# Kernel optimization log

Measured on AMD Instinct MI355X. Metric: run time of the kernel, lower is better.

## Reference

```python
import jax, jax.numpy as jnp
import numpy as np

D_MODEL = 768
H = 12
D_FF = 3072
EPS = 1e-6


def _layernorm(x, alpha, bias):
    # torch.std default is Bessel-corrected (ddof=1); denom is (std + eps)
    mean = jnp.mean(x, axis=-1, keepdims=True)
    var = jnp.sum((x - mean) ** 2, axis=-1, keepdims=True) / (x.shape[-1] - 1)
    std = jnp.sqrt(var)
    return alpha * (x - mean) / (std + EPS) + bias


def _linear(x, w, b):
    # torch nn.Linear: y = x @ W.T + b, W is [out, in]
    return jnp.einsum('...i,oi->...o', x, w) + b


def setup_inputs() -> dict:
    key = jax.random.key(0)
    ks = jax.random.split(key, 16)
    B, S = 8, 1024
    sc = 1.0 / np.sqrt(D_MODEL)
    inp = {
        'x': jax.random.normal(ks[0], (B, S, D_MODEL), dtype=jnp.float32),
        'mask': jax.random.randint(ks[1], (B, 1, 1, S), 0, 2, dtype=jnp.int32),
        'wq': jax.random.normal(ks[2], (D_MODEL, D_MODEL), dtype=jnp.float32) * sc,
        'bq': jnp.zeros((D_MODEL,), jnp.float32),
        'wk': jax.random.normal(ks[3], (D_MODEL, D_MODEL), dtype=jnp.float32) * sc,
        'bk': jnp.zeros((D_MODEL,), jnp.float32),
        'wv': jax.random.normal(ks[4], (D_MODEL, D_MODEL), dtype=jnp.float32) * sc,
        'bv': jnp.zeros((D_MODEL,), jnp.float32),
        'wo': jax.random.normal(ks[5], (D_MODEL, D_MODEL), dtype=jnp.float32) * sc,
        'bo': jnp.zeros((D_MODEL,), jnp.float32),
        'ln1_a': jnp.ones((D_MODEL,), jnp.float32),
        'ln1_b': jnp.zeros((D_MODEL,), jnp.float32),
        'ln2_a': jnp.ones((D_MODEL,), jnp.float32),
        'ln2_b': jnp.zeros((D_MODEL,), jnp.float32),
        'w1': jax.random.normal(ks[6], (D_FF, D_MODEL), dtype=jnp.float32) * sc,
        'b1': jnp.zeros((D_FF,), jnp.float32),
        'w2': jax.random.normal(ks[7], (D_MODEL, D_FF), dtype=jnp.float32) * (1.0 / np.sqrt(D_FF)),
        'b2': jnp.zeros((D_MODEL,), jnp.float32),
    }
    return inp


def reference(x, mask, wq, bq, wk, bk, wv, bv, wo, bo,
              ln1_a, ln1_b, ln2_a, ln2_b, w1, b1, w2, b2):
    B, S, _ = x.shape
    d_k = D_MODEL // H

    # --- residual 1: pre-LN self-attention (dropout identity at eval) ---
    xn = _layernorm(x, ln1_a, ln1_b)
    q = _linear(xn, wq, bq).reshape(B, S, H, d_k).transpose(0, 2, 1, 3)
    k = _linear(xn, wk, bk).reshape(B, S, H, d_k).transpose(0, 2, 1, 3)
    v = _linear(xn, wv, bv).reshape(B, S, H, d_k).transpose(0, 2, 1, 3)

    scores = jnp.einsum('bhqd,bhkd->bhqk', q, k) / jnp.sqrt(jnp.float32(d_k))
    # faithful quirk: masked positions set to 1e-9, NOT -inf
    scores = jnp.where(mask == 0, jnp.float32(1e-9), scores)
    attn = jax.nn.softmax(scores, axis=-1)
    ctx = jnp.einsum('bhqk,bhkd->bhqd', attn, v)
    ctx = ctx.transpose(0, 2, 1, 3).reshape(B, S, D_MODEL)
    x = x + _linear(ctx, wo, bo)

    # --- residual 2: pre-LN feed-forward ---
    xn = _layernorm(x, ln2_a, ln2_b)
    ff = _linear(jax.nn.relu(_linear(xn, w1, b1)), w2, b2)
    return x + ff
```

## Files before the change

### kernel.cpp

```cpp
#include <hip/hip_runtime.h>
#include <stdint.h>

#define D_MODEL 768
#define D_FF    3072
#define NH      12
#define DK      64
#define BB      8
#define SS      1024
#define NTOK    (BB*SS)
#define QST     2304

typedef float          f32x4  __attribute__((ext_vector_type(4)));
typedef __bf16         bf16x8 __attribute__((ext_vector_type(8)));
typedef unsigned short us8v   __attribute__((ext_vector_type(8)));
typedef unsigned short us4v   __attribute__((ext_vector_type(4)));

__device__ __forceinline__ unsigned short f2b(float f) {
  unsigned int u = __builtin_bit_cast(unsigned int, f);
  u = (u + 0x7fffu + ((u >> 16) & 1u)) >> 16;
  return (unsigned short)u;
}
__device__ __forceinline__ float b2f(unsigned short h) {
  unsigned int u = ((unsigned int)h) << 16;
  return __builtin_bit_cast(float, u);
}
__device__ __forceinline__ float exp2a(float x) {
  float r; asm("v_exp_f32 %0, %1" : "=v"(r) : "v"(x)); return r;
}
__device__ __forceinline__ unsigned int cvtpk(float lo, float hi) {
  unsigned int r;
  asm("v_cvt_pk_bf16_f32 %0, %1, %2" : "=v"(r) : "v"(lo), "v"(hi));
  return r;
}

#define N4TOT 1769472
__global__ __launch_bounds__(256) void cast6_kernel(
    const float* __restrict__ s0, const float* __restrict__ s1,
    const float* __restrict__ s2, const float* __restrict__ s3,
    const float* __restrict__ s4, const float* __restrict__ s5,
    unsigned short* __restrict__ d0, unsigned short* __restrict__ d1,
    unsigned short* __restrict__ d2, unsigned short* __restrict__ d3,
    unsigned short* __restrict__ d4, unsigned short* __restrict__ d5) {
  int i = blockIdx.x * 256 + threadIdx.x;
  if (i >= N4TOT) return;
  const float* src; unsigned short* dst; int off;
  if (i < 147456)       { src = s0; dst = d0; off = i; }
  else if (i < 294912)  { src = s1; dst = d1; off = i - 147456; }
  else if (i < 442368)  { src = s2; dst = d2; off = i - 294912; }
  else if (i < 589824)  { src = s3; dst = d3; off = i - 442368; }
  else if (i < 1179648) { src = s4; dst = d4; off = i - 589824; }
  else                  { src = s5; dst = d5; off = i - 1179648; }
  float4 f = ((const float4*)src)[off];
  us4v o; o.x = f2b(f.x); o.y = f2b(f.y); o.z = f2b(f.z); o.w = f2b(f.w);
  *(us4v*)(dst + (size_t)off * 4) = o;
}

__global__ __launch_bounds__(256) void ln_kernel(const float* __restrict__ x,
                                                 const float* __restrict__ ga,
                                                 const float* __restrict__ gb,
                                                 unsigned short* __restrict__ y) {
  int row = blockIdx.x;
  const float* xr = x + (size_t)row * D_MODEL;
  int t = threadIdx.x, w = t >> 6, l = t & 63;
  float v0 = xr[t], v1 = xr[t + 256], v2 = xr[t + 512];
  float s = v0 + v1 + v2;
  #pragma unroll
  for (int off = 32; off; off >>= 1) s += __shfl_xor(s, off);
  __shared__ float red[4];
  __shared__ float stats[2];
  if (l == 0) red[w] = s;
  __syncthreads();
  if (t == 0) stats[0] = (red[0] + red[1] + red[2] + red[3]) * (1.0f / 768.0f);
  __syncthreads();
  float mean = stats[0];
  float d0 = v0 - mean, d1 = v1 - mean, d2 = v2 - mean;
  float ss = d0 * d0 + d1 * d1 + d2 * d2;
  #pragma unroll
  for (int off = 32; off; off >>= 1) ss += __shfl_xor(ss, off);
  __syncthreads();
  if (l == 0) red[w] = ss;
  __syncthreads();
  if (t == 0) {
    float tot = red[0] + red[1] + red[2] + red[3];
    stats[1] = 1.0f / (sqrtf(tot * (1.0f / 767.0f)) + 1e-6f);
  }
  __syncthreads();
  float inv = stats[1];
  unsigned short* yr = y + (size_t)row * D_MODEL;
  yr[t]       = f2b(ga[t]       * (d0 * inv) + gb[t]);
  yr[t + 256] = f2b(ga[t + 256] * (d1 * inv) + gb[t + 256]);
  yr[t + 512] = f2b(ga[t + 512] * (d2 * inv) + gb[t + 512]);
}

#define GLDS(g, l) __builtin_amdgcn_global_load_lds( \
    (__attribute__((address_space(1))) const void*)(g), \
    (__attribute__((address_space(3))) void*)(l), 16, 0, 0)

template<int BN>
__global__ __launch_bounds__(256) void gemm_t(
    const unsigned short* __restrict__ A,
    const unsigned short* __restrict__ W,
    const float* __restrict__ biasA,
    const float* __restrict__ biasB,
    const float* __restrict__ biasC,
    int segw,
    const float* __restrict__ resid,
    float* __restrict__ outF,
    unsigned short* __restrict__ outB,
    int M, int N, int K, int relu) {
  constexpr int BK  = (BN == 128) ? 32 : 64;
  constexpr int WC  = (BN == 128) ? 2 : 1;
  constexpr int MF  = (BN == 128) ? 4 : 2;
  constexpr int NF  = 4;
  constexpr int ASZ = 128 * BK;
  constexpr int BSZ = BN * BK;
  __shared__ unsigned short As[2 * ASZ];
  __shared__ unsigned short Bs[2 * BSZ];
  int t = threadIdx.x;
  int w = t >> 6, l = t & 63;
  int brow = blockIdx.x * 128;
  int bcol = blockIdx.y * BN;
  int wr = (w / WC) * (MF * 16);
  int wc = (w % WC) * (NF * 16);

  const unsigned short *ga0, *ga1, *gb0, *gb1;
  if constexpr (BN == 128) {
    ga0 = A + (size_t)(brow + (t >> 2)) * K + (t & 3) * 8;
    ga1 = ga0 + (size_t)64 * K;
    gb0 = W + (size_t)(bcol + (t >> 2)) * K + (t & 3) * 8;
    gb1 = gb0 + (size_t)64 * K;
  } else {
    int r5 = t >> 3;
    int swz = (t & 7) ^ (r5 & 7);
    ga0 = A + (size_t)(brow + r5) * K + swz * 8;
    gb0 = W + (size_t)(bcol + r5) * K + swz * 8;
    ga1 = gb1 = nullptr;
  }

  f32x4 acc[MF][NF];
  #pragma unroll
  for (int m = 0; m < MF; m++)
    #pragma unroll
    for (int n = 0; n < NF; n++)
      acc[m][n] = (f32x4){0.f, 0.f, 0.f, 0.f};

  int arow = wr + (l & 15);
  int bcw  = wc + (l & 15);
  int g    = l >> 4;
  int kk   = g * 8;
  const int nt = K / BK;

  auto stage = [&](int ti, int buf) {
    int k0 = ti * BK;
    if constexpr (BN == 128) {
      GLDS(ga0 + k0, As + buf * ASZ + t * 8);
      GLDS(ga1 + k0, As + buf * ASZ + 2048 + t * 8);
      GLDS(gb0 + k0, Bs + buf * BSZ + t * 8);
      GLDS(gb1 + k0, Bs + buf * BSZ + 2048 + t * 8);
    } else {
      #pragma unroll
      for (int i = 0; i < 4; i++)
        GLDS(ga0 + k0 + (size_t)(32 * i) * K, As + buf * ASZ + i * 2048 + t * 8);
      #pragma unroll
      for (int i = 0; i < 2; i++)
        GLDS(gb0 + k0 + (size_t)(32 * i) * K, Bs + buf * BSZ + i * 2048 + t * 8);
    }
  };

  stage(0, 0);
  __syncthreads();

  int cb = 0;
  for (int ti = 0; ti < nt; ti++) {
    if (ti + 1 < nt) stage(ti + 1, cb ^ 1);
    #pragma unroll
    for (int h = 0; h < BK / 32; h++) {
      bf16x8 af[MF], bfv[NF];
      #pragma unroll
      for (int m = 0; m < MF; m++) {
        int aro = arow + m * 16;
        if constexpr (BN == 128)
          af[m] = *(const bf16x8*)(As + cb * ASZ + aro * 32 + kk);
        else
          af[m] = *(const bf16x8*)(As + cb * ASZ + aro * 64 +
                                   ((((h << 2) + g) ^ (l & 7)) << 3));
      }
      #pragma unroll
      for (int n = 0; n < NF; n++) {
        int bco = bcw + n * 16;
        if constexpr (BN == 128)
          bfv[n] = *(const bf16x8*)(Bs + cb * BSZ + bco * 32 + kk);
        else
          bfv[n] = *(const bf16x8*)(Bs + cb * BSZ + bco * 64 +
                                    ((((h << 2) + g) ^ (l & 7)) << 3));
      }
      #pragma unroll
      for (int m = 0; m < MF; m++)
        #pragma unroll
        for (int n = 0; n < NF; n++)
          acc[m][n] = __builtin_amdgcn_mfma_f32_16x16x32_bf16(af[m], bfv[n], acc[m][n], 0, 0, 0);
    }
    if (ti + 1 < nt) __syncthreads();
    cb ^= 1;
  }

  #pragma unroll
  for (int n = 0; n < NF; n++) {
    int col = bcol + wc + n * 16 + (l & 15);
    int seg = col / segw, off = col - seg * segw;
    const float* bp = (seg == 0) ? biasA : ((seg == 1) ? biasB : biasC);
    float bv = bp[off];
    #pragma unroll
    for (int m = 0; m < MF; m++) {
      int row0 = brow + wr + m * 16 + (l >> 4) * 4;
      #pragma unroll
      for (int r = 0; r < 4; r++) {
        int row = row0 + r;
        float vacc = acc[m][n][r] + bv;
        if (resid) vacc += resid[(size_t)row * N + col];
        if (relu)  vacc = fmaxf(vacc, 0.f);
        if (outF)  outF[(size_t)row * N + col] = vacc;
        if (outB)  outB[(size_t)row * N + col] = f2b(vacc);
      }
    }
  }
}

#define PPAD 72
#define KPAD 72
#define SM_C1 0.18033688011112043f
#define SM_C2 1.4426950408889634e-9f

__global__ __launch_bounds__(256) void attn_mfma(
    const unsigned short* __restrict__ qkv,
    const int* __restrict__ mask,
    unsigned short* __restrict__ ctx) {
  int bh = blockIdx.x;
  int qt = blockIdx.y;
  int b = bh / NH, h = bh % NH;
  int t = threadIdx.x, w = t >> 6, l = t & 63;
  int ql = l & 15, g = l >> 4;

  const unsigned short* kp = qkv + 768 + h * DK;
  const unsigned short* vp = qkv + 1536 + h * DK;

  __shared__ unsigned short Ks[4096];
  __shared__ unsigned short Vt[64 * KPAD];
  __shared__ unsigned short Ps[128 * PPAD];
  __shared__ float mk01[64];
  __shared__ float corrw[4][2][16];
  __shared__ float lrw[4][2][16];

  int srow = t >> 3;
  int sblk = t & 7;
  int sb0  = sblk ^ (srow & 7);
  int sb1  = sblk ^ ((srow + 32) & 7);

  bf16x8 qf[2][2];
  {
    const unsigned short* qp = qkv + h * DK;
    size_t row0 = (size_t)(b * SS + qt * 128 + w * 32 + ql);
    #pragma unroll
    for (int s = 0; s < 2; s++)
      #pragma unroll
      for (int ks = 0; ks < 2; ks++)
        qf[s][ks] = *(const bf16x8*)(qp + (row0 + s * 16) * QST + ks * 32 + g * 8);
  }

  f32x4 acc_o[2][4];
  #pragma unroll
  for (int s = 0; s < 2; s++)
    #pragma unroll
    for (int nf = 0; nf < 4; nf++) acc_o[s][nf] = (f32x4){0.f, 0.f, 0.f, 0.f};
  float mrun[2] = {-INFINITY, -INFINITY};
  float lrun[2] = {0.f, 0.f};

  for (int kt = 0; kt < 16; kt++) {
    size_t tok0 = (size_t)(b * SS + kt * 64);
    GLDS(kp + (tok0 + srow)      * QST + sb0 * 8, Ks + t * 8);
    GLDS(kp + (tok0 + srow + 32) * QST + sb1 * 8, Ks + 2048 + t * 8);
    {
      const unsigned short* vsrc = vp + (tok0 + l) * QST + w * 16;
      us8v v0 = *(const us8v*)vsrc;
      us8v v1 = *(const us8v*)(vsrc + 8);
      #pragma unroll
      for (int j = 0; j < 8; j++) {
        Vt[(w * 16 + j)     * KPAD + l] = v0[j];
        Vt[(w * 16 + 8 + j) * KPAD + l] = v1[j];
      }
    }
    if (t < 64) mk01[t] = mask[b * SS + kt * 64 + t] ? 1.0f : 0.0f;
    __syncthreads();

    f32x4 sa[2][4];
    #pragma unroll
    for (int s = 0; s < 2; s++)
      #pragma unroll
      for (int kf = 0; kf < 4; kf++) sa[s][kf] = (f32x4){0.f, 0.f, 0.f, 0.f};
    #pragma unroll
    for (int ks = 0; ks < 2; ks++) {
      bf16x8 kfr[4];
      #pragma unroll
      for (int kf = 0; kf < 4; kf++) {
        int row = kf * 16 + ql;
        kfr[kf] = *(const bf16x8*)(Ks + row * 64 + ((g + 4 * ks) ^ (ql & 7)) * 8);
      }
      #pragma unroll
      for (int s = 0; s < 2; s++)
        #pragma unroll
        for (int kf = 0; kf < 4; kf++)
          sa[s][kf] = __builtin_amdgcn_mfma_f32_16x16x32_bf16(kfr[kf], qf[s][ks], sa[s][kf], 0, 0, 0);
    }

    #pragma unroll
    for (int s = 0; s < 2; s++) {
      float pv[16];
      float tm = -INFINITY;
      #pragma unroll
      for (int kf = 0; kf < 4; kf++)
        #pragma unroll
        for (int r = 0; r < 4; r++) {
          float m01 = mk01[kf * 16 + g * 4 + r];
          float xm = sa[s][kf][r] * SM_C1 - SM_C2;
          float sc = fmaf(m01, xm, SM_C2);
          pv[kf * 4 + r] = sc;
          tm = fmaxf(tm, sc);
        }
      tm = fmaxf(tm, __shfl_xor(tm, 16));
      tm = fmaxf(tm, __shfl_xor(tm, 32));
      float mn = fmaxf(mrun[s], tm);
      float corr = exp2a(mrun[s] - mn);
      float rs = 0.f;
      #pragma unroll
      for (int i = 0; i < 16; i++) { pv[i] = exp2a(pv[i] - mn); rs += pv[i]; }
      rs += __shfl_xor(rs, 16);
      rs += __shfl_xor(rs, 32);
      mrun[s] = mn;
      lrun[s] = lrun[s] * corr + rs;

      int prow = w * 32 + s * 16 + ql;
      #pragma unroll
      for (int kf = 0; kf < 4; kf++) {
        uint2 pk;
        pk.x = cvtpk(pv[kf * 4 + 0], pv[kf * 4 + 1]);
        pk.y = cvtpk(pv[kf * 4 + 2], pv[kf * 4 + 3]);
        *(uint2*)(Ps + prow * PPAD + kf * 16 + g * 4) = pk;
      }
      if (l < 16) corrw[w][s][l] = corr;
    }

    #pragma unroll
    for (int s = 0; s < 2; s++) {
      float cb0 = corrw[w][s][g * 4 + 0], cb1 = corrw[w][s][g * 4 + 1];
      float cb2 = corrw[w][s][g * 4 + 2], cb3 = corrw[w][s][g * 4 + 3];
      #pragma unroll
      for (int nf = 0; nf < 4; nf++) {
        acc_o[s][nf][0] *= cb0; acc_o[s][nf][1] *= cb1;
        acc_o[s][nf][2] *= cb2; acc_o[s][nf][3] *= cb3;
      }
    }
    #pragma unroll
    for (int ks = 0; ks < 2; ks++) {
      bf16x8 vfr[4];
      #pragma unroll
      for (int nf = 0; nf < 4; nf++)
        vfr[nf] = *(const bf16x8*)(Vt + (ql + nf * 16) * KPAD + g * 8 + ks * 32);
      #pragma unroll
      for (int s = 0; s < 2; s++) {
        bf16x8 pa = *(const bf16x8*)(Ps + (w * 32 + s * 16 + ql) * PPAD + g * 8 + ks * 32);
        #pragma unroll
        for (int nf = 0; nf < 4; nf++)
          acc_o[s][nf] = __builtin_amdgcn_mfma_f32_16x16x32_bf16(pa, vfr[nf], acc_o[s][nf], 0, 0, 0);
      }
    }
    __syncthreads();
  }

  #pragma unroll
  for (int s = 0; s < 2; s++)
    if (l < 16) lrw[w][s][l] = lrun[s];
  #pragma unroll
  for (int s = 0; s < 2; s++) {
    float li0 = 1.0f / lrw[w][s][g * 4 + 0], li1 = 1.0f / lrw[w][s][g * 4 + 1];
    float li2 = 1.0f / lrw[w][s][g * 4 + 2], li3 = 1.0f / lrw[w][s][g * 4 + 3];
    #pragma unroll
    for (int nf = 0; nf < 4; nf++) {
      #pragma unroll
      for (int r = 0; r < 4; r++) {
        float li = (r == 0) ? li0 : (r == 1) ? li1 : (r == 2) ? li2 : li3;
        int tok = b * SS + qt * 128 + w * 32 + s * 16 + g * 4 + r;
        ctx[(size_t)tok * D_MODEL + h * DK + nf * 16 + ql] = f2b(acc_o[s][nf][r] * li);
      }
    }
  }
}

extern "C" void kernel_launch(void* const* d_in, const int* in_sizes, int n_in,
                              void* d_out, int out_size, void* d_ws, size_t ws_size,
                              hipStream_t stream) {
  const float* x    = (const float*)d_in[0];
  const int*   mask = (const int*)d_in[1];
  const float* wq   = (const float*)d_in[2];
  const float* bq   = (const float*)d_in[3];
  const float* wk   = (const float*)d_in[4];
  const float* bk   = (const float*)d_in[5];
  const float* wv   = (const float*)d_in[6];
  const float* bv   = (const float*)d_in[7];
  const float* wo   = (const float*)d_in[8];
  const float* bo   = (const float*)d_in[9];
  const float* ln1a = (const float*)d_in[10];
  const float* ln1b = (const float*)d_in[11];
  const float* ln2a = (const float*)d_in[12];
  const float* ln2b = (const float*)d_in[13];
  const float* w1   = (const float*)d_in[14];
  const float* b1   = (const float*)d_in[15];
  const float* w2   = (const float*)d_in[16];
  const float* b2   = (const float*)d_in[17];

  char* ws = (char*)d_ws;
  unsigned short* wqkvb = (unsigned short*)(ws + 0);
  unsigned short* wob   = (unsigned short*)(ws + 3538944);
  unsigned short* w1b   = (unsigned short*)(ws + 4718592);
  unsigned short* w2b   = (unsigned short*)(ws + 9437184);
  unsigned short* xnb   = (unsigned short*)(ws + 14155776);
  unsigned short* qkvb  = (unsigned short*)(ws + 26738688);
  unsigned short* ctxb  = (unsigned short*)(ws + 64487424);
  float*          x1    = (float*)(ws + 26738688);
  unsigned short* h1b   = (unsigned short*)(ws + 51904512);

  cast6_kernel<<<N4TOT / 256, 256, 0, stream>>>(
      wq, wk, wv, wo, w1, w2,
      wqkvb, wqkvb + 589824, wqkvb + 1179648, wob, w1b, w2b);

  ln_kernel<<<NTOK, 256, 0, stream>>>(x, ln1a, ln1b, xnb);

  dim3 gqkv(NTOK / 128, QST / 128);
  gemm_t<128><<<gqkv, 256, 0, stream>>>(xnb, wqkvb, bq, bk, bv, 768,
                                        nullptr, nullptr, qkvb,
                                        NTOK, QST, D_MODEL, 0);

  dim3 ga(BB * NH, SS / 128);
  attn_mfma<<<ga, 256, 0, stream>>>(qkvb, mask, ctxb);

  dim3 gwo(NTOK / 128, D_MODEL / 64);
  gemm_t<64><<<gwo, 256, 0, stream>>>(ctxb, wob, bo, nullptr, nullptr, D_MODEL,
                                      x, x1, nullptr,
                                      NTOK, D_MODEL, D_MODEL, 0);

  ln_kernel<<<NTOK, 256, 0, stream>>>(x1, ln2a, ln2b, xnb);

  dim3 gff(NTOK / 128, D_FF / 128);
  gemm_t<128><<<gff, 256, 0, stream>>>(xnb, w1b, b1, nullptr, nullptr, D_FF,
                                       nullptr, nullptr, h1b,
                                       NTOK, D_FF, D_MODEL, 1);

  dim3 gff2(NTOK / 128, D_MODEL / 64);
  gemm_t<64><<<gff2, 256, 0, stream>>>(h1b, w2b, b2, nullptr, nullptr, D_MODEL,
                                       x1, (float*)d_out, nullptr,
                                       NTOK, D_MODEL, D_FF, 0);
}
```

Before: 278.9 us.

## Double-buffer K tiles, prefetch V/mask, and add lazy softmax rescaling in attention

The attention kernel now double-buffers the K tile in shared memory. It prefetches the next K tile (async global-to-LDS), the next V rows and the next mask values into registers while the current tile is computed, so global-load latency overlaps with MFMA work. The online softmax skips the running-max update and output rescale unless some row's new max exceeds the old one by more than a threshold. Correction and final normalisation factors are now broadcast with wave shuffles instead of shared-memory arrays. This costs more LDS and registers per block, and the lazy rescale relies on the skipped-update window staying small enough to avoid overflow in exp2.

```diff
diff --git a/kernel.cpp b/kernel.cpp
--- a/kernel.cpp
+++ b/kernel.cpp
@@ -244,12 +244,10 @@
   const unsigned short* kp = qkv + 768 + h * DK;
   const unsigned short* vp = qkv + 1536 + h * DK;
 
-  __shared__ unsigned short Ks[4096];
+  __shared__ unsigned short Ks[2][4096];
   __shared__ unsigned short Vt[64 * KPAD];
   __shared__ unsigned short Ps[128 * PPAD];
   __shared__ float mk01[64];
-  __shared__ float corrw[4][2][16];
-  __shared__ float lrw[4][2][16];
 
   int srow = t >> 3;
   int sblk = t & 7;
@@ -267,6 +265,19 @@
         qf[s][ks] = *(const bf16x8*)(qp + (row0 + s * 16) * QST + ks * 32 + g * 8);
   }
 
+  {
+    size_t tok0 = (size_t)(b * SS);
+    GLDS(kp + (tok0 + srow) * QST + sb0 * 8, &Ks[0][t * 8]);
+    GLDS(kp + (tok0 + srow + 32) * QST + sb1 * 8, &Ks[0][2048 + t * 8]);
+  }
+  us8v vA, vB;
+  {
+    const unsigned short* vs = vp + ((size_t)(b * SS) + l) * QST + w * 16;
+    vA = *(const us8v*)vs;
+    vB = *(const us8v*)(vs + 8);
+  }
+  float mkreg = mask[b * SS + (t & 63)] ? 1.0f : 0.0f;
+
   f32x4 acc_o[2][4];
   #pragma unroll
   for (int s = 0; s < 2; s++)
@@ -275,22 +286,25 @@
   float mrun[2] = {-INFINITY, -INFINITY};
   float lrun[2] = {0.f, 0.f};
 
+  int cur = 0;
   for (int kt = 0; kt < 16; kt++) {
-    size_t tok0 = (size_t)(b * SS + kt * 64);
-    GLDS(kp + (tok0 + srow)      * QST + sb0 * 8, Ks + t * 8);
-    GLDS(kp + (tok0 + srow + 32) * QST + sb1 * 8, Ks + 2048 + t * 8);
-    {
-      const unsigned short* vsrc = vp + (tok0 + l) * QST + w * 16;
-      us8v v0 = *(const us8v*)vsrc;
-      us8v v1 = *(const us8v*)(vsrc + 8);
-      #pragma unroll
-      for (int j = 0; j < 8; j++) {
-        Vt[(w * 16 + j)     * KPAD + l] = v0[j];
-        Vt[(w * 16 + 8 + j) * KPAD + l] = v1[j];
-      }
-    }
-    if (t < 64) mk01[t] = mask[b * SS + kt * 64 + t] ? 1.0f : 0.0f;
+    #pragma unroll
+    for (int j = 0; j < 8; j++) {
+      Vt[(w * 16 + j)     * KPAD + l] = vA[j];
+      Vt[(w * 16 + 8 + j) * KPAD + l] = vB[j];
+    }
+    if (t < 64) mk01[t] = mkreg;
     __syncthreads();
+
+    if (kt + 1 < 16) {
+      size_t tn = (size_t)(b * SS + (kt + 1) * 64);
+      GLDS(kp + (tn + srow) * QST + sb0 * 8, &Ks[cur ^ 1][t * 8]);
+      GLDS(kp + (tn + srow + 32) * QST + sb1 * 8, &Ks[cur ^ 1][2048 + t * 8]);
+      const unsigned short* vs2 = vp + (tn + l) * QST + w * 16;
+      vA = *(const us8v*)vs2;
+      vB = *(const us8v*)(vs2 + 8);
+      mkreg = mask[b * SS + (kt + 1) * 64 + (t & 63)] ? 1.0f : 0.0f;
+    }
 
     f32x4 sa[2][4];
     #pragma unroll
@@ -303,7 +317,7 @@
       #pragma unroll
       for (int kf = 0; kf < 4; kf++) {
         int row = kf * 16 + ql;
-        kfr[kf] = *(const bf16x8*)(Ks + row * 64 + ((g + 4 * ks) ^ (ql & 7)) * 8);
+        kfr[kf] = *(const bf16x8*)(&Ks[cur][row * 64 + ((g + 4 * ks) ^ (ql & 7)) * 8]);
       }
       #pragma unroll
       for (int s = 0; s < 2; s++)
@@ -312,6 +326,13 @@
           sa[s][kf] = __builtin_amdgcn_mfma_f32_16x16x32_bf16(kfr[kf], qf[s][ks], sa[s][kf], 0, 0, 0);
     }
 
+    float m01v[16];
+    #pragma unroll
+    for (int kf = 0; kf < 4; kf++)
+      #pragma unroll
+      for (int r = 0; r < 4; r++)
+        m01v[kf * 4 + r] = mk01[kf * 16 + g * 4 + r];
+
     #pragma unroll
     for (int s = 0; s < 2; s++) {
       float pv[16];
@@ -320,23 +341,35 @@
       for (int kf = 0; kf < 4; kf++)
         #pragma unroll
         for (int r = 0; r < 4; r++) {
-          float m01 = mk01[kf * 16 + g * 4 + r];
           float xm = sa[s][kf][r] * SM_C1 - SM_C2;
-          float sc = fmaf(m01, xm, SM_C2);
+          float sc = fmaf(m01v[kf * 4 + r], xm, SM_C2);
           pv[kf * 4 + r] = sc;
           tm = fmaxf(tm, sc);
         }
       tm = fmaxf(tm, __shfl_xor(tm, 16));
       tm = fmaxf(tm, __shfl_xor(tm, 32));
-      float mn = fmaxf(mrun[s], tm);
-      float corr = exp2a(mrun[s] - mn);
+      bool renorm = !__all(tm <= mrun[s] + 8.0f);
+      if (renorm) {
+        float mn = fmaxf(mrun[s], tm);
+        float corr = exp2a(mrun[s] - mn);
+        mrun[s] = mn;
+        lrun[s] *= corr;
+        float c0 = __shfl(corr, (l & 48) | (g * 4 + 0));
+        float c1 = __shfl(corr, (l & 48) | (g * 4 + 1));
+        float c2 = __shfl(corr, (l & 48) | (g * 4 + 2));
+        float c3 = __shfl(corr, (l & 48) | (g * 4 + 3));
+        #pragma unroll
+        for (int nf = 0; nf < 4; nf++) {
+          acc_o[s][nf][0] *= c0; acc_o[s][nf][1] *= c1;
+          acc_o[s][nf][2] *= c2; acc_o[s][nf][3] *= c3;
+        }
+      }
       float rs = 0.f;
       #pragma unroll
-      for (int i = 0; i < 16; i++) { pv[i] = exp2a(pv[i] - mn); rs += pv[i]; }
+      for (int i = 0; i < 16; i++) { pv[i] = exp2a(pv[i] - mrun[s]); rs += pv[i]; }
       rs += __shfl_xor(rs, 16);
       rs += __shfl_xor(rs, 32);
-      mrun[s] = mn;
-      lrun[s] = lrun[s] * corr + rs;
+      lrun[s] += rs;
 
       int prow = w * 32 + s * 16 + ql;
       #pragma unroll
@@ -346,19 +379,8 @@
         pk.y = cvtpk(pv[kf * 4 + 2], pv[kf * 4 + 3]);
         *(uint2*)(Ps + prow * PPAD + kf * 16 + g * 4) = pk;
       }
-      if (l < 16) corrw[w][s][l] = corr;
-    }
-
-    #pragma unroll
-    for (int s = 0; s < 2; s++) {
-      float cb0 = corrw[w][s][g * 4 + 0], cb1 = corrw[w][s][g * 4 + 1];
-      float cb2 = corrw[w][s][g * 4 + 2], cb3 = corrw[w][s][g * 4 + 3];
-      #pragma unroll
-      for (int nf = 0; nf < 4; nf++) {
-        acc_o[s][nf][0] *= cb0; acc_o[s][nf][1] *= cb1;
-        acc_o[s][nf][2] *= cb2; acc_o[s][nf][3] *= cb3;
-      }
-    }
+    }
+
     #pragma unroll
     for (int ks = 0; ks < 2; ks++) {
       bf16x8 vfr[4];
@@ -374,15 +396,15 @@
       }
     }
     __syncthreads();
-  }
-
-  #pragma unroll
-  for (int s = 0; s < 2; s++)
-    if (l < 16) lrw[w][s][l] = lrun[s];
+    cur ^= 1;
+  }
+
   #pragma unroll
   for (int s = 0; s < 2; s++) {
-    float li0 = 1.0f / lrw[w][s][g * 4 + 0], li1 = 1.0f / lrw[w][s][g * 4 + 1];
-    float li2 = 1.0f / lrw[w][s][g * 4 + 2], li3 = 1.0f / lrw[w][s][g * 4 + 3];
+    float li0 = 1.0f / __shfl(lrun[s], (l & 48) | (g * 4 + 0));
+    float li1 = 1.0f / __shfl(lrun[s], (l & 48) | (g * 4 + 1));
+    float li2 = 1.0f / __shfl(lrun[s], (l & 48) | (g * 4 + 2));
+    float li3 = 1.0f / __shfl(lrun[s], (l & 48) | (g * 4 + 3));
     #pragma unroll
     for (int nf = 0; nf < 4; nf++) {
       #pragma unroll
```

Measured after the change: 283.8 us. Within noise of the previous version (+1.8%).

## Split attention block across 8 waves with 16 query rows each

Applied to the files above, without the earlier changes.

The attention kernel now launches 512 threads per block. Each of 8 waves handles 16 query rows instead of 4 waves handling 32, and the K/V tile loads are spread over twice as many threads. This halves per-wave register state (accumulators, score fragments) and raises wave count, aiming for better latency hiding. The cost is that each wave reloads the same K and V fragments from LDS for half the MFMA work, and the block barriers now span more waves.

```diff
diff --git a/kernel.cpp b/kernel.cpp
--- a/kernel.cpp
+++ b/kernel.cpp
@@ -231,7 +231,7 @@
 #define SM_C1 0.18033688011112043f
 #define SM_C2 1.4426950408889634e-9f
 
-__global__ __launch_bounds__(256) void attn_mfma(
+__global__ __launch_bounds__(512) void attn_mfma(
     const unsigned short* __restrict__ qkv,
     const int* __restrict__ mask,
     unsigned short* __restrict__ ctx) {
@@ -248,55 +248,43 @@
   __shared__ unsigned short Vt[64 * KPAD];
   __shared__ unsigned short Ps[128 * PPAD];
   __shared__ float mk01[64];
-  __shared__ float corrw[4][2][16];
-  __shared__ float lrw[4][2][16];
+  __shared__ float corrw[8][16];
+  __shared__ float lrw[8][16];
 
   int srow = t >> 3;
-  int sblk = t & 7;
-  int sb0  = sblk ^ (srow & 7);
-  int sb1  = sblk ^ ((srow + 32) & 7);
-
-  bf16x8 qf[2][2];
+  int sb0  = (t & 7) ^ (srow & 7);
+  int vkey = t & 63, vd = (t >> 6) * 8;
+
+  bf16x8 qf[2];
   {
     const unsigned short* qp = qkv + h * DK;
-    size_t row0 = (size_t)(b * SS + qt * 128 + w * 32 + ql);
-    #pragma unroll
-    for (int s = 0; s < 2; s++)
-      #pragma unroll
-      for (int ks = 0; ks < 2; ks++)
-        qf[s][ks] = *(const bf16x8*)(qp + (row0 + s * 16) * QST + ks * 32 + g * 8);
-  }
-
-  f32x4 acc_o[2][4];
-  #pragma unroll
-  for (int s = 0; s < 2; s++)
-    #pragma unroll
-    for (int nf = 0; nf < 4; nf++) acc_o[s][nf] = (f32x4){0.f, 0.f, 0.f, 0.f};
-  float mrun[2] = {-INFINITY, -INFINITY};
-  float lrun[2] = {0.f, 0.f};
+    size_t row0 = (size_t)(b * SS + qt * 128 + w * 16 + ql);
+    #pragma unroll
+    for (int ks = 0; ks < 2; ks++)
+      qf[ks] = *(const bf16x8*)(qp + row0 * QST + ks * 32 + g * 8);
+  }
+
+  f32x4 acc_o[4];
+  #pragma unroll
+  for (int nf = 0; nf < 4; nf++) acc_o[nf] = (f32x4){0.f, 0.f, 0.f, 0.f};
+  float mrun = -INFINITY, lrun = 0.f;
 
   for (int kt = 0; kt < 16; kt++) {
     size_t tok0 = (size_t)(b * SS + kt * 64);
-    GLDS(kp + (tok0 + srow)      * QST + sb0 * 8, Ks + t * 8);
-    GLDS(kp + (tok0 + srow + 32) * QST + sb1 * 8, Ks + 2048 + t * 8);
     {
-      const unsigned short* vsrc = vp + (tok0 + l) * QST + w * 16;
+      const unsigned short* vsrc = vp + (tok0 + vkey) * QST + vd;
       us8v v0 = *(const us8v*)vsrc;
-      us8v v1 = *(const us8v*)(vsrc + 8);
-      #pragma unroll
-      for (int j = 0; j < 8; j++) {
-        Vt[(w * 16 + j)     * KPAD + l] = v0[j];
-        Vt[(w * 16 + 8 + j) * KPAD + l] = v1[j];
-      }
+      GLDS(kp + (tok0 + srow) * QST + sb0 * 8, Ks + t * 8);
+      #pragma unroll
+      for (int j = 0; j < 8; j++)
+        Vt[(vd + j) * KPAD + vkey] = v0[j];
     }
     if (t < 64) mk01[t] = mask[b * SS + kt * 64 + t] ? 1.0f : 0.0f;
     __syncthreads();
 
-    f32x4 sa[2][4];
-    #pragma unroll
-    for (int s = 0; s < 2; s++)
-      #pragma unroll
-      for (int kf = 0; kf < 4; kf++) sa[s][kf] = (f32x4){0.f, 0.f, 0.f, 0.f};
+    f32x4 sa[4];
+    #pragma unroll
+    for (int kf = 0; kf < 4; kf++) sa[kf] = (f32x4){0.f, 0.f, 0.f, 0.f};
     #pragma unroll
     for (int ks = 0; ks < 2; ks++) {
       bf16x8 kfr[4];
@@ -306,57 +294,51 @@
         kfr[kf] = *(const bf16x8*)(Ks + row * 64 + ((g + 4 * ks) ^ (ql & 7)) * 8);
       }
       #pragma unroll
-      for (int s = 0; s < 2; s++)
-        #pragma unroll
-        for (int kf = 0; kf < 4; kf++)
-          sa[s][kf] = __builtin_amdgcn_mfma_f32_16x16x32_bf16(kfr[kf], qf[s][ks], sa[s][kf], 0, 0, 0);
-    }
-
-    #pragma unroll
-    for (int s = 0; s < 2; s++) {
-      float pv[16];
-      float tm = -INFINITY;
-      #pragma unroll
       for (int kf = 0; kf < 4; kf++)
-        #pragma unroll
-        for (int r = 0; r < 4; r++) {
-          float m01 = mk01[kf * 16 + g * 4 + r];
-          float xm = sa[s][kf][r] * SM_C1 - SM_C2;
-          float sc = fmaf(m01, xm, SM_C2);
-          pv[kf * 4 + r] = sc;
-          tm = fmaxf(tm, sc);
-        }
-      tm = fmaxf(tm, __shfl_xor(tm, 16));
-      tm = fmaxf(tm, __shfl_xor(tm, 32));
-      float mn = fmaxf(mrun[s], tm);
-      float corr = exp2a(mrun[s] - mn);
-      float rs = 0.f;
-      #pragma unroll
-      for (int i = 0; i < 16; i++) { pv[i] = exp2a(pv[i] - mn); rs += pv[i]; }
-      rs += __shfl_xor(rs, 16);
-      rs += __shfl_xor(rs, 32);
-      mrun[s] = mn;
-      lrun[s] = lrun[s] * corr + rs;
-
-      int prow = w * 32 + s * 16 + ql;
-      #pragma unroll
-      for (int kf = 0; kf < 4; kf++) {
-        uint2 pk;
-        pk.x = cvtpk(pv[kf * 4 + 0], pv[kf * 4 + 1]);
-        pk.y = cvtpk(pv[kf * 4 + 2], pv[kf * 4 + 3]);
-        *(uint2*)(Ps + prow * PPAD + kf * 16 + g * 4) = pk;
-      }
-      if (l < 16) corrw[w][s][l] = corr;
-    }
-
-    #pragma unroll
-    for (int s = 0; s < 2; s++) {
-      float cb0 = corrw[w][s][g * 4 + 0], cb1 = corrw[w][s][g * 4 + 1];
-      float cb2 = corrw[w][s][g * 4 + 2], cb3 = corrw[w][s][g * 4 + 3];
+        sa[kf] = __builtin_amdgcn_mfma_f32_16x16x32_bf16(kfr[kf], qf[ks], sa[kf], 0, 0, 0);
+    }
+
+    float pv[16];
+    float tm = -INFINITY;
+    #pragma unroll
+    for (int kf = 0; kf < 4; kf++)
+      #pragma unroll
+      for (int r = 0; r < 4; r++) {
+        float m01 = mk01[kf * 16 + g * 4 + r];
+        float xm = sa[kf][r] * SM_C1 - SM_C2;
+        float sc = fmaf(m01, xm, SM_C2);
+        pv[kf * 4 + r] = sc;
+        tm = fmaxf(tm, sc);
+      }
+    tm = fmaxf(tm, __shfl_xor(tm, 16));
+    tm = fmaxf(tm, __shfl_xor(tm, 32));
+    float mn = fmaxf(mrun, tm);
+    float corr = exp2a(mrun - mn);
+    float rs = 0.f;
+    #pragma unroll
+    for (int i = 0; i < 16; i++) { pv[i] = exp2a(pv[i] - mn); rs += pv[i]; }
+    rs += __shfl_xor(rs, 16);
+    rs += __shfl_xor(rs, 32);
+    mrun = mn;
+    lrun = lrun * corr + rs;
+
+    int prow = w * 16 + ql;
+    #pragma unroll
+    for (int kf = 0; kf < 4; kf++) {
+      uint2 pk;
+      pk.x = cvtpk(pv[kf * 4 + 0], pv[kf * 4 + 1]);
+      pk.y = cvtpk(pv[kf * 4 + 2], pv[kf * 4 + 3]);
+      *(uint2*)(Ps + prow * PPAD + kf * 16 + g * 4) = pk;
+    }
+    if (l < 16) corrw[w][l] = corr;
+
+    {
+      float cb0 = corrw[w][g * 4 + 0], cb1 = corrw[w][g * 4 + 1];
+      float cb2 = corrw[w][g * 4 + 2], cb3 = corrw[w][g * 4 + 3];
       #pragma unroll
       for (int nf = 0; nf < 4; nf++) {
-        acc_o[s][nf][0] *= cb0; acc_o[s][nf][1] *= cb1;
-        acc_o[s][nf][2] *= cb2; acc_o[s][nf][3] *= cb3;
+        acc_o[nf][0] *= cb0; acc_o[nf][1] *= cb1;
+        acc_o[nf][2] *= cb2; acc_o[nf][3] *= cb3;
       }
     }
     #pragma unroll
@@ -365,32 +347,24 @@
       #pragma unroll
       for (int nf = 0; nf < 4; nf++)
         vfr[nf] = *(const bf16x8*)(Vt + (ql + nf * 16) * KPAD + g * 8 + ks * 32);
-      #pragma unroll
-      for (int s = 0; s < 2; s++) {
-        bf16x8 pa = *(const bf16x8*)(Ps + (w * 32 + s * 16 + ql) * PPAD + g * 8 + ks * 32);
-        #pragma unroll
-        for (int nf = 0; nf < 4; nf++)
-          acc_o[s][nf] = __builtin_amdgcn_mfma_f32_16x16x32_bf16(pa, vfr[nf], acc_o[s][nf], 0, 0, 0);
-      }
+      bf16x8 pa = *(const bf16x8*)(Ps + prow * PPAD + g * 8 + ks * 32);
+      #pragma unroll
+      for (int nf = 0; nf < 4; nf++)
+        acc_o[nf] = __builtin_amdgcn_mfma_f32_16x16x32_bf16(pa, vfr[nf], acc_o[nf], 0, 0, 0);
     }
     __syncthreads();
   }
 
-  #pragma unroll
-  for (int s = 0; s < 2; s++)
-    if (l < 16) lrw[w][s][l] = lrun[s];
-  #pragma unroll
-  for (int s = 0; s < 2; s++) {
-    float li0 = 1.0f / lrw[w][s][g * 4 + 0], li1 = 1.0f / lrw[w][s][g * 4 + 1];
-    float li2 = 1.0f / lrw[w][s][g * 4 + 2], li3 = 1.0f / lrw[w][s][g * 4 + 3];
-    #pragma unroll
-    for (int nf = 0; nf < 4; nf++) {
-      #pragma unroll
-      for (int r = 0; r < 4; r++) {
-        float li = (r == 0) ? li0 : (r == 1) ? li1 : (r == 2) ? li2 : li3;
-        int tok = b * SS + qt * 128 + w * 32 + s * 16 + g * 4 + r;
-        ctx[(size_t)tok * D_MODEL + h * DK + nf * 16 + ql] = f2b(acc_o[s][nf][r] * li);
-      }
+  if (l < 16) lrw[w][l] = lrun;
+  float li0 = 1.0f / lrw[w][g * 4 + 0], li1 = 1.0f / lrw[w][g * 4 + 1];
+  float li2 = 1.0f / lrw[w][g * 4 + 2], li3 = 1.0f / lrw[w][g * 4 + 3];
+  #pragma unroll
+  for (int nf = 0; nf < 4; nf++) {
+    #pragma unroll
+    for (int r = 0; r < 4; r++) {
+      float li = (r == 0) ? li0 : (r == 1) ? li1 : (r == 2) ? li2 : li3;
+      int tok = b * SS + qt * 128 + w * 16 + g * 4 + r;
+      ctx[(size_t)tok * D_MODEL + h * DK + nf * 16 + ql] = f2b(acc_o[nf][r] * li);
     }
   }
 }
@@ -440,7 +414,7 @@
                                         NTOK, QST, D_MODEL, 0);
 
   dim3 ga(BB * NH, SS / 128);
-  attn_mfma<<<ga, 256, 0, stream>>>(qkvb, mask, ctxb);
+  attn_mfma<<<ga, 512, 0, stream>>>(qkvb, mask, ctxb);
 
   dim3 gwo(NTOK / 128, D_MODEL / 64);
   gemm_t<64><<<gwo, 256, 0, stream>>>(ctxb, wob, bo, nullptr, nullptr, D_MODEL,
```

Result: no change. 281.1 us (+0.8%).
